# Optimization experiments

Measured on AMD Instinct MI355X. Metric: run time of the kernel, lower is better.

## Reference

```python
import jax, jax.numpy as jnp
import numpy as np

N = 200000      # query points
D_IN = 3        # coordinate dims
H = 256         # hidden features
L = 4           # hidden layers (between first and last Perceptron)
S = 8           # n_series == out_features


def setup_inputs() -> dict:
    key = jax.random.key(0)
    ks = jax.random.split(key, 7)
    coords = jax.random.normal(ks[0], (N, D_IN), dtype=jnp.float32)
    # Stacked per-series weights (all series share shapes; original loads the
    # same checkpoint into each, but we use independent random params).
    scale0 = 1.0 / np.sqrt(D_IN)
    scaleh = 1.0 / np.sqrt(H)
    W0 = jax.random.uniform(ks[1], (S, D_IN, H), jnp.float32, -scale0, scale0)
    b0 = jax.random.uniform(ks[2], (S, H), jnp.float32, -scale0, scale0)
    Wh = jax.random.uniform(ks[3], (S, L, H, H), jnp.float32, -scaleh, scaleh)
    bh = jax.random.uniform(ks[4], (S, L, H), jnp.float32, -scaleh, scaleh)
    Wout = jax.random.uniform(ks[5], (S, H, 1), jnp.float32, -scaleh, scaleh)
    bout = jax.random.uniform(ks[6], (S, 1), jnp.float32, -scaleh, scaleh)
    return {"coords": coords, "W0": W0, "b0": b0, "Wh": Wh, "bh": bh,
            "Wout": Wout, "bout": bout}


def reference(coords, W0, b0, Wh, bh, Wout, bout):
    # All S series' MLPs batched into grouped GEMMs (einsum over series axis s).
    # Perceptron = Linear + softplus; last layer is plain Linear.
    h = jax.nn.softplus(jnp.einsum('nd,sdh->snh', coords, W0) + b0[:, None, :])
    for i in range(L):  # small fixed layer count
        h = jax.nn.softplus(
            jnp.einsum('snh,shk->snk', h, Wh[:, i]) + bh[:, i][:, None, :])
    out = jnp.einsum('snh,sho->sno', h, Wout) + bout[:, None, :]  # [S,N,1]
    output = jnp.transpose(out[..., 0], (1, 0))  # concat along dim=1 -> [N,S]
    return (output, coords)
```

## Files before the change

kernel.cpp:

```cpp
#include <hip/hip_runtime.h>
#include <hip/hip_bf16.h>
#include <cstdint>

typedef __attribute__((ext_vector_type(8))) short short8;
typedef __attribute__((ext_vector_type(4))) float float4v;

#define LOG2E 1.44269504088896340736f
#define LN2   0.69314718055994530942f

#if __has_builtin(__builtin_amdgcn_exp2f)
__device__ __forceinline__ float fexp2(float x){ return __builtin_amdgcn_exp2f(x); }
#else
__device__ __forceinline__ float fexp2(float x){ return exp2f(x); }
#endif
#if __has_builtin(__builtin_amdgcn_logf)
__device__ __forceinline__ float flog2(float x){ return __builtin_amdgcn_logf(x); }
#else
__device__ __forceinline__ float flog2(float x){ return log2f(x); }
#endif

__device__ __forceinline__ float softplus_hat(float zh){
  return flog2(1.0f + fexp2(zh));
}

__device__ __forceinline__ unsigned short bf16_trunc(float f){
  return (unsigned short)(__builtin_bit_cast(unsigned int, f) >> 16);
}

__global__ void convert_wh(const float* __restrict__ Wh,
                           unsigned short* __restrict__ Wt){
  int e = blockIdx.x * 256 + threadIdx.x;
  int n  = e & 255;
  int k  = (e >> 8) & 255;
  int sl = e >> 16;
  float v = Wh[e];
  __hip_bfloat16 h = __float2bfloat16(v);
  Wt[(sl << 16) + ((k >> 5) << 13) + (n << 5) + (k & 31)] =
      __builtin_bit_cast(unsigned short, h);
}

__device__ __forceinline__ void layer_mfma(
    const unsigned short* __restrict__ slab,
    const unsigned short* __restrict__ h_lds,
    int lane, int colb, int q, float4v acc[4][4])
{
  const unsigned short* bbase = slab + (colb << 5) + (q << 3);

  short8 bq[3][4];
  #pragma unroll
  for (int i = 0; i < 3; ++i)
    #pragma unroll
    for (int ni = 0; ni < 4; ++ni)
      bq[i][ni] = *(const short8*)(bbase + (i << 13) + (ni << 9));

  short8 a0[4], a1[4];
  #pragma unroll
  for (int mi = 0; mi < 4; ++mi) {
    int m = mi * 16 + (lane & 15);
    a0[mi] = *(const short8*)&h_lds[m * 256 + ((q ^ (m & 7)) << 3)];
  }

  #pragma unroll
  for (int kb = 0; kb < 8; ++kb) {
    short8* cur = (kb & 1) ? a1 : a0;
    short8* nxt = (kb & 1) ? a0 : a1;
    if (kb < 7) {
      #pragma unroll
      for (int mi = 0; mi < 4; ++mi) {
        int m = mi * 16 + (lane & 15);
        int o = ((kb + 1) << 2) + q;
        nxt[mi] = *(const short8*)&h_lds[m * 256 + ((o ^ (m & 7)) << 3)];
      }
    }
    #pragma unroll
    for (int mi = 0; mi < 4; ++mi)
      #pragma unroll
      for (int ni = 0; ni < 4; ++ni)
        acc[mi][ni] = __builtin_amdgcn_mfma_f32_16x16x32_bf16(
            cur[mi], bq[kb % 3][ni], acc[mi][ni], 0, 0, 0);
    if (kb + 3 < 8) {
      #pragma unroll
      for (int ni = 0; ni < 4; ++ni)
        bq[kb % 3][ni] = *(const short8*)(bbase + ((kb + 3) << 13) + (ni << 9));
    }
  }
}

__global__ __launch_bounds__(256, 2) void series_mlp(
    const float* __restrict__ coords,
    const float* __restrict__ W0, const float* __restrict__ b0,
    const float* __restrict__ bh,
    const float* __restrict__ Wout, const float* __restrict__ bout,
    const unsigned short* __restrict__ Wt,
    float* __restrict__ out)
{
  __shared__ __align__(16) unsigned short h_lds[64 * 256];
  __shared__ float cbuf[192];

  const int tid  = threadIdx.x;
  const int lane = tid & 63;
  const int wave = tid >> 6;
  const int s    = blockIdx.x & 7;
  const int m0   = (blockIdx.x >> 3) * 64;

  if (tid < 192) cbuf[tid] = coords[m0 * 3 + tid];
  __syncthreads();

  {
    const int c  = tid;
    const float w0 = W0[(s * 3 + 0) * 256 + c] * LOG2E;
    const float w1 = W0[(s * 3 + 1) * 256 + c] * LOG2E;
    const float w2 = W0[(s * 3 + 2) * 256 + c] * LOG2E;
    const float bb = b0[s * 256 + c] * LOG2E;
    const int cc = c >> 3, cl = c & 7;
    for (int m = 0; m < 64; ++m) {
      float zh = fmaf(cbuf[m * 3 + 2], w2,
                 fmaf(cbuf[m * 3 + 1], w1,
                 fmaf(cbuf[m * 3 + 0], w0, bb)));
      h_lds[m * 256 + ((cc ^ (m & 7)) << 3) + cl] = bf16_trunc(softplus_hat(zh));
    }
  }
  __syncthreads();

  const int colb = (wave << 6) + (lane & 15);
  const int q    = lane >> 4;

  #pragma unroll
  for (int l = 0; l < 3; ++l) {
    const unsigned short* slab = Wt + (((s << 2) + l) << 16);

    float bias[4];
    #pragma unroll
    for (int ni = 0; ni < 4; ++ni)
      bias[ni] = bh[((s << 2) + l) * 256 + colb + ni * 16] * LOG2E;

    float4v acc[4][4];
    #pragma unroll
    for (int mi = 0; mi < 4; ++mi)
      #pragma unroll
      for (int ni = 0; ni < 4; ++ni)
        acc[mi][ni] = (float4v){bias[ni], bias[ni], bias[ni], bias[ni]};

    layer_mfma(slab, h_lds, lane, colb, q, acc);

    #pragma unroll
    for (int mi = 0; mi < 4; ++mi)
      #pragma unroll
      for (int ni = 0; ni < 4; ++ni) {
        float4v v = acc[mi][ni];
        #pragma unroll
        for (int r = 0; r < 4; ++r) v[r] = softplus_hat(v[r]);
        acc[mi][ni] = v;
      }

    __syncthreads();

    #pragma unroll
    for (int mi = 0; mi < 4; ++mi) {
      #pragma unroll
      for (int ni = 0; ni < 4; ++ni) {
        float4v v = acc[mi][ni];
        int col = (wave << 6) + ni * 16 + (lane & 15);
        int cc = col >> 3, cl = col & 7;
        int mb = mi * 16 + (q << 2);
        #pragma unroll
        for (int r = 0; r < 4; ++r) {
          int m = mb + r;
          h_lds[m * 256 + ((cc ^ (m & 7)) << 3) + cl] = bf16_trunc(v[r]);
        }
      }
    }
    __syncthreads();
  }

  {
    const unsigned short* slab = Wt + (((s << 2) + 3) << 16);

    float bias[4];
    #pragma unroll
    for (int ni = 0; ni < 4; ++ni)
      bias[ni] = bh[((s << 2) + 3) * 256 + colb + ni * 16] * LOG2E;

    float4v acc[4][4];
    #pragma unroll
    for (int mi = 0; mi < 4; ++mi)
      #pragma unroll
      for (int ni = 0; ni < 4; ++ni)
        acc[mi][ni] = (float4v){bias[ni], bias[ni], bias[ni], bias[ni]};

    layer_mfma(slab, h_lds, lane, colb, q, acc);

    float wv[4];
    #pragma unroll
    for (int ni = 0; ni < 4; ++ni)
      wv[ni] = Wout[(s << 8) + colb + ni * 16];
    float p[16];
    #pragma unroll
    for (int i = 0; i < 16; ++i) p[i] = 0.f;
    #pragma unroll
    for (int mi = 0; mi < 4; ++mi)
      #pragma unroll
      for (int ni = 0; ni < 4; ++ni) {
        float4v v = acc[mi][ni];
        #pragma unroll
        for (int r = 0; r < 4; ++r)
          p[mi * 4 + r] = fmaf(softplus_hat(v[r]), wv[ni], p[mi * 4 + r]);
      }

    __syncthreads();
    float* red = (float*)h_lds;
    #pragma unroll
    for (int mi = 0; mi < 4; ++mi)
      #pragma unroll
      for (int r = 0; r < 4; ++r) {
        int row = mi * 16 + (q << 2) + r;
        red[row * 68 + (wave << 4) + (lane & 15)] = p[mi * 4 + r];
      }
    __syncthreads();

    if (tid < 64) {
      const float4v* rr = (const float4v*)&red[tid * 68];
      float4v a = rr[0];
      #pragma unroll
      for (int i = 1; i < 16; ++i) {
        float4v b = rr[i];
        a.x += b.x; a.y += b.y; a.z += b.z; a.w += b.w;
      }
      float tot = (a.x + a.y) + (a.z + a.w);
      out[(m0 + tid) * 8 + s] = fmaf(LN2, tot, bout[s]);
    }
  }
}

__global__ __launch_bounds__(256) void series_mlp_slow(
    const float* __restrict__ coords,
    const float* __restrict__ W0, const float* __restrict__ b0,
    const float* __restrict__ Wh, const float* __restrict__ bh,
    const float* __restrict__ Wout, const float* __restrict__ bout,
    float* __restrict__ out)
{
  __shared__ float h[64 * 256];
  __shared__ float cbuf[192];
  __shared__ float red[256];
  const int tid = threadIdx.x;
  const int s   = blockIdx.y;
  const int m0  = blockIdx.x * 64;

  if (tid < 192) cbuf[tid] = coords[m0 * 3 + tid];
  __syncthreads();
  {
    const float w0 = W0[(s * 3 + 0) * 256 + tid];
    const float w1 = W0[(s * 3 + 1) * 256 + tid];
    const float w2 = W0[(s * 3 + 2) * 256 + tid];
    const float bb = b0[s * 256 + tid];
    for (int m = 0; m < 64; ++m) {
      float z = fmaf(cbuf[m * 3 + 2], w2,
                fmaf(cbuf[m * 3 + 1], w1,
                fmaf(cbuf[m * 3 + 0], w0, bb)));
      h[m * 256 + tid] = LN2 * softplus_hat(z * LOG2E);
    }
  }
  __syncthreads();

  for (int l = 0; l < 4; ++l) {
    const float* W = Wh + (((s << 2) + l) << 16);
    const float bb = bh[((s << 2) + l) * 256 + tid];
    float acc[64];
    #pragma unroll
    for (int m = 0; m < 64; ++m) acc[m] = bb;
    for (int kc = 0; kc < 64; ++kc) {
      float w0 = W[(kc * 4 + 0) * 256 + tid];
      float w1 = W[(kc * 4 + 1) * 256 + tid];
      float w2 = W[(kc * 4 + 2) * 256 + tid];
      float w3 = W[(kc * 4 + 3) * 256 + tid];
      #pragma unroll
      for (int m = 0; m < 64; ++m) {
        float4v hv = *(const float4v*)&h[m * 256 + kc * 4];
        acc[m] = fmaf(hv.w, w3, fmaf(hv.z, w2,
                 fmaf(hv.y, w1, fmaf(hv.x, w0, acc[m]))));
      }
    }
    __syncthreads();
    #pragma unroll
    for (int m = 0; m < 64; ++m)
      h[m * 256 + tid] = LN2 * softplus_hat(acc[m] * LOG2E);
    __syncthreads();
  }
  {
    const int m = tid >> 2, qq = tid & 3;
    const float* wv = Wout + (s << 8);
    float sum = 0.f;
    for (int i = 0; i < 16; ++i) {
      int kk = (qq << 6) + ((((tid & 15) + i) << 2) & 63);
      float4v hv = *(const float4v*)&h[m * 256 + kk];
      sum += hv.x * wv[kk] + hv.y * wv[kk + 1] + hv.z * wv[kk + 2] + hv.w * wv[kk + 3];
    }
    red[tid] = sum;
    __syncthreads();
    if (tid < 64)
      out[(m0 + tid) * 8 + s] =
          red[tid * 4] + red[tid * 4 + 1] + red[tid * 4 + 2] + red[tid * 4 + 3] + bout[s];
  }
}

extern "C" void kernel_launch(void* const* d_in, const int* in_sizes, int n_in,
                              void* d_out, int out_size, void* d_ws, size_t ws_size,
                              hipStream_t stream) {
  const float* coords = (const float*)d_in[0];
  const float* W0     = (const float*)d_in[1];
  const float* b0     = (const float*)d_in[2];
  const float* Wh     = (const float*)d_in[3];
  const float* bh     = (const float*)d_in[4];
  const float* Wout   = (const float*)d_in[5];
  const float* bout   = (const float*)d_in[6];
  float* out = (float*)d_out;

  const size_t WT_BYTES = (size_t)8 * 4 * 256 * 256 * 2;
  if (ws_size >= WT_BYTES) {
    unsigned short* Wt = (unsigned short*)d_ws;
    convert_wh<<<8192, 256, 0, stream>>>(Wh, Wt);
    series_mlp<<<dim3(25000), dim3(256), 0, stream>>>(
        coords, W0, b0, bh, Wout, bout, Wt, out);
  } else {
    series_mlp_slow<<<dim3(3125, 8), dim3(256), 0, stream>>>(
        coords, W0, b0, Wh, bh, Wout, bout, out);
  }
  hipMemcpyAsync(out + (size_t)200000 * 8, coords,
                 (size_t)200000 * 3 * sizeof(float),
                 hipMemcpyDeviceToDevice, stream);
}
```

Before: 1.001 ms.

## Prefetch next layer weights across layers and pad LDS rows instead of XOR swizzle

The weight register ring buffer now persists across hidden layers, so the first three k-blocks of the next layer's weights are loaded during the tail of the current layer's MFMA loop. This hides the global-load latency at each layer start. The XOR-swizzled LDS activation layout is replaced by a padded row stride of 264 elements, which simplifies address arithmetic to constant offsets. The first layer also reads coordinates as float4 vectors. The risks are different LDS bank-conflict behaviour under padding, slightly more LDS use, and higher register pressure from keeping prefetched weights live across layer boundaries.

Measured after the change: 916.0 us. 1.09x faster.

```diff
diff --git a/kernel.cpp b/kernel.cpp
--- a/kernel.cpp
+++ b/kernel.cpp
@@ -27,6 +27,8 @@
   return (unsigned short)(__builtin_bit_cast(unsigned int, f) >> 16);
 }
 
+#define HSTRIDE 264
+
 __global__ void convert_wh(const float* __restrict__ Wh,
                            unsigned short* __restrict__ Wt){
   int e = blockIdx.x * 256 + threadIdx.x;
@@ -39,26 +41,23 @@
       __builtin_bit_cast(unsigned short, h);
 }
 
-__device__ __forceinline__ void layer_mfma(
-    const unsigned short* __restrict__ slab,
-    const unsigned short* __restrict__ h_lds,
-    int lane, int colb, int q, float4v acc[4][4])
+__device__ __forceinline__ float4v bf16_mfma(short8 a, short8 b, float4v c){
+  return __builtin_amdgcn_mfma_f32_16x16x32_bf16(a, b, c, 0, 0, 0);
+}
+
+template<int L>
+__device__ __forceinline__ void hidden_mfma(
+    const unsigned short* __restrict__ bbase0,
+    const unsigned short* __restrict__ aptr,
+    short8 (&bq)[3][4], float4v (&acc)[4][4])
 {
-  const unsigned short* bbase = slab + (colb << 5) + (q << 3);
-
-  short8 bq[3][4];
-  #pragma unroll
-  for (int i = 0; i < 3; ++i)
-    #pragma unroll
-    for (int ni = 0; ni < 4; ++ni)
-      bq[i][ni] = *(const short8*)(bbase + (i << 13) + (ni << 9));
+  const unsigned short* bb = bbase0 + L * 65536;
+  const unsigned short* bn = bbase0 + (L + 1) * 65536;
 
   short8 a0[4], a1[4];
   #pragma unroll
-  for (int mi = 0; mi < 4; ++mi) {
-    int m = mi * 16 + (lane & 15);
-    a0[mi] = *(const short8*)&h_lds[m * 256 + ((q ^ (m & 7)) << 3)];
-  }
+  for (int mi = 0; mi < 4; ++mi)
+    a0[mi] = *(const short8*)(aptr + mi * 4224);
 
   #pragma unroll
   for (int kb = 0; kb < 8; ++kb) {
@@ -66,22 +65,23 @@
     short8* nxt = (kb & 1) ? a0 : a1;
     if (kb < 7) {
       #pragma unroll
-      for (int mi = 0; mi < 4; ++mi) {
-        int m = mi * 16 + (lane & 15);
-        int o = ((kb + 1) << 2) + q;
-        nxt[mi] = *(const short8*)&h_lds[m * 256 + ((o ^ (m & 7)) << 3)];
-      }
-    }
+      for (int mi = 0; mi < 4; ++mi)
+        nxt[mi] = *(const short8*)(aptr + mi * 4224 + (kb + 1) * 32);
+    }
+    const int slot = (8 * L + kb) % 3;
     #pragma unroll
     for (int mi = 0; mi < 4; ++mi)
       #pragma unroll
       for (int ni = 0; ni < 4; ++ni)
-        acc[mi][ni] = __builtin_amdgcn_mfma_f32_16x16x32_bf16(
-            cur[mi], bq[kb % 3][ni], acc[mi][ni], 0, 0, 0);
-    if (kb + 3 < 8) {
+        acc[mi][ni] = bf16_mfma(cur[mi], bq[slot][ni], acc[mi][ni]);
+    if (kb < 5) {
       #pragma unroll
       for (int ni = 0; ni < 4; ++ni)
-        bq[kb % 3][ni] = *(const short8*)(bbase + ((kb + 3) << 13) + (ni << 9));
+        bq[slot][ni] = *(const short8*)(bb + (kb + 3) * 8192 + ni * 512);
+    } else if (L < 3) {
+      #pragma unroll
+      for (int ni = 0; ni < 4; ++ni)
+        bq[slot][ni] = *(const short8*)(bn + (kb - 5) * 8192 + ni * 512);
     }
   }
 }
@@ -94,7 +94,7 @@
     const unsigned short* __restrict__ Wt,
     float* __restrict__ out)
 {
-  __shared__ __align__(16) unsigned short h_lds[64 * 256];
+  __shared__ __align__(16) unsigned short h_lds[64 * HSTRIDE];
   __shared__ float cbuf[192];
 
   const int tid  = threadIdx.x;
@@ -112,83 +112,91 @@
     const float w1 = W0[(s * 3 + 1) * 256 + c] * LOG2E;
     const float w2 = W0[(s * 3 + 2) * 256 + c] * LOG2E;
     const float bb = b0[s * 256 + c] * LOG2E;
-    const int cc = c >> 3, cl = c & 7;
-    for (int m = 0; m < 64; ++m) {
-      float zh = fmaf(cbuf[m * 3 + 2], w2,
-                 fmaf(cbuf[m * 3 + 1], w1,
-                 fmaf(cbuf[m * 3 + 0], w0, bb)));
-      h_lds[m * 256 + ((cc ^ (m & 7)) << 3) + cl] = bf16_trunc(softplus_hat(zh));
+    const float4v* c4 = (const float4v*)cbuf;
+    #pragma unroll
+    for (int j = 0; j < 16; ++j) {
+      float4v x0 = c4[j * 3 + 0];
+      float4v x1 = c4[j * 3 + 1];
+      float4v x2 = c4[j * 3 + 2];
+      float z0 = fmaf(x0.z, w2, fmaf(x0.y, w1, fmaf(x0.x, w0, bb)));
+      float z1 = fmaf(x1.y, w2, fmaf(x1.x, w1, fmaf(x0.w, w0, bb)));
+      float z2 = fmaf(x2.x, w2, fmaf(x1.w, w1, fmaf(x1.z, w0, bb)));
+      float z3 = fmaf(x2.w, w2, fmaf(x2.z, w1, fmaf(x2.y, w0, bb)));
+      h_lds[(4 * j + 0) * HSTRIDE + c] = bf16_trunc(softplus_hat(z0));
+      h_lds[(4 * j + 1) * HSTRIDE + c] = bf16_trunc(softplus_hat(z1));
+      h_lds[(4 * j + 2) * HSTRIDE + c] = bf16_trunc(softplus_hat(z2));
+      h_lds[(4 * j + 3) * HSTRIDE + c] = bf16_trunc(softplus_hat(z3));
     }
   }
   __syncthreads();
 
   const int colb = (wave << 6) + (lane & 15);
   const int q    = lane >> 4;
-
+  const unsigned short* aptr = h_lds + (lane & 15) * HSTRIDE + q * 8;
+  unsigned short* cptr = h_lds + (q * 4) * HSTRIDE + colb;
+
+  const unsigned short* bbase0 = Wt + ((s << 2) << 16) + (colb << 5) + (q << 3);
+
+  short8 bq[3][4];
   #pragma unroll
-  for (int l = 0; l < 3; ++l) {
-    const unsigned short* slab = Wt + (((s << 2) + l) << 16);
-
+  for (int i = 0; i < 3; ++i)
+    #pragma unroll
+    for (int ni = 0; ni < 4; ++ni)
+      bq[i][ni] = *(const short8*)(bbase0 + i * 8192 + ni * 512);
+
+  float4v acc[4][4];
+
+  #define HIDDEN_LAYER(L)                                                     \
+  {                                                                           \
+    float bias[4];                                                            \
+    _Pragma("unroll")                                                         \
+    for (int ni = 0; ni < 4; ++ni)                                            \
+      bias[ni] = bh[((s << 2) + L) * 256 + colb + ni * 16] * LOG2E;           \
+    _Pragma("unroll")                                                         \
+    for (int mi = 0; mi < 4; ++mi)                                            \
+      _Pragma("unroll")                                                       \
+      for (int ni = 0; ni < 4; ++ni)                                          \
+        acc[mi][ni] = (float4v){bias[ni], bias[ni], bias[ni], bias[ni]};      \
+    hidden_mfma<L>(bbase0, aptr, bq, acc);                                    \
+    _Pragma("unroll")                                                         \
+    for (int mi = 0; mi < 4; ++mi)                                            \
+      _Pragma("unroll")                                                       \
+      for (int ni = 0; ni < 4; ++ni) {                                        \
+        float4v v = acc[mi][ni];                                              \
+        _Pragma("unroll")                                                     \
+        for (int r = 0; r < 4; ++r) v[r] = softplus_hat(v[r]);                \
+        acc[mi][ni] = v;                                                      \
+      }                                                                       \
+    __syncthreads();                                                          \
+    _Pragma("unroll")                                                         \
+    for (int mi = 0; mi < 4; ++mi)                                            \
+      _Pragma("unroll")                                                       \
+      for (int ni = 0; ni < 4; ++ni) {                                        \
+        float4v v = acc[mi][ni];                                              \
+        _Pragma("unroll")                                                     \
+        for (int r = 0; r < 4; ++r)                                           \
+          cptr[mi * 4224 + r * HSTRIDE + ni * 16] = bf16_trunc(v[r]);         \
+      }                                                                       \
+    __syncthreads();                                                          \
+  }
+
+  HIDDEN_LAYER(0)
+  HIDDEN_LAYER(1)
+  HIDDEN_LAYER(2)
+  #undef HIDDEN_LAYER
+
+  {
     float bias[4];
     #pragma unroll
     for (int ni = 0; ni < 4; ++ni)
-      bias[ni] = bh[((s << 2) + l) * 256 + colb + ni * 16] * LOG2E;
-
-    float4v acc[4][4];
+      bias[ni] = bh[((s << 2) + 3) * 256 + colb + ni * 16] * LOG2E;
     #pragma unroll
     for (int mi = 0; mi < 4; ++mi)
       #pragma unroll
       for (int ni = 0; ni < 4; ++ni)
         acc[mi][ni] = (float4v){bias[ni], bias[ni], bias[ni], bias[ni]};
 
-    layer_mfma(slab, h_lds, lane, colb, q, acc);
-
-    #pragma unroll
-    for (int mi = 0; mi < 4; ++mi)
-      #pragma unroll
-      for (int ni = 0; ni < 4; ++ni) {
-        float4v v = acc[mi][ni];
-        #pragma unroll
-        for (int r = 0; r < 4; ++r) v[r] = softplus_hat(v[r]);
-        acc[mi][ni] = v;
-      }
-
-    __syncthreads();
-
-    #pragma unroll
-    for (int mi = 0; mi < 4; ++mi) {
-      #pragma unroll
-      for (int ni = 0; ni < 4; ++ni) {
-        float4v v = acc[mi][ni];
-        int col = (wave << 6) + ni * 16 + (lane & 15);
-        int cc = col >> 3, cl = col & 7;
-        int mb = mi * 16 + (q << 2);
-        #pragma unroll
-        for (int r = 0; r < 4; ++r) {
-          int m = mb + r;
-          h_lds[m * 256 + ((cc ^ (m & 7)) << 3) + cl] = bf16_trunc(v[r]);
-        }
-      }
-    }
-    __syncthreads();
-  }
-
-  {
-    const unsigned short* slab = Wt + (((s << 2) + 3) << 16);
-
-    float bias[4];
-    #pragma unroll
-    for (int ni = 0; ni < 4; ++ni)
-      bias[ni] = bh[((s << 2) + 3) * 256 + colb + ni * 16] * LOG2E;
-
-    float4v acc[4][4];
-    #pragma unroll
-    for (int mi = 0; mi < 4; ++mi)
-      #pragma unroll
-      for (int ni = 0; ni < 4; ++ni)
-        acc[mi][ni] = (float4v){bias[ni], bias[ni], bias[ni], bias[ni]};
-
-    layer_mfma(slab, h_lds, lane, colb, q, acc);
+    hidden_mfma<3>(bbase0, aptr, bq, acc);
 
     float wv[4];
     #pragma unroll
```

## Ping-pong two row tiles per block to overlap MFMA with softplus epilogue

Applied to the files above, without the earlier changes.

Each block now owns two 64-row tiles held in two LDS buffers. Each phase runs one tile's layer GEMM while applying softplus and the bf16 store, or the output dot product, to the other tile's accumulators, so transcendental work interleaves with MFMA issue. The weight prefetch ring now runs continuously across layer boundaries, and the LDS activation layout changes from an XOR-swizzled row-major layout to a chunk-major one. The grid is halved, one tile is computed twice, and register pressure doubles because two accumulator sets stay live.

Measured after the change: 947.0 us. -5.4%, faster.

```diff
diff --git a/kernel.cpp b/kernel.cpp
--- a/kernel.cpp
+++ b/kernel.cpp
@@ -39,26 +39,37 @@
       __builtin_bit_cast(unsigned short, h);
 }
 
-__device__ __forceinline__ void layer_mfma(
-    const unsigned short* __restrict__ slab,
-    const unsigned short* __restrict__ h_lds,
-    int lane, int colb, int q, float4v acc[4][4])
+__device__ __forceinline__ float4v bf16_mfma(short8 a, short8 b, float4v c){
+  return __builtin_amdgcn_mfma_f32_16x16x32_bf16(a, b, c, 0, 0, 0);
+}
+
+template<int P>
+__device__ __forceinline__ void run_phase(
+    const unsigned short* __restrict__ bbase0,
+    const unsigned short* __restrict__ aS,
+    unsigned short* __restrict__ cO,
+    short8 (&bq)[3][4],
+    float4v (&accS)[4][4], float4v (&accO)[4][4],
+    const float* __restrict__ bh_s, int colb,
+    const float (&wv)[4], float (&pd)[16])
 {
-  const unsigned short* bbase = slab + (colb << 5) + (q << 3);
-
-  short8 bq[3][4];
-  #pragma unroll
-  for (int i = 0; i < 3; ++i)
+  constexpr int LYR = P >> 1;
+  {
+    float bias[4];
     #pragma unroll
     for (int ni = 0; ni < 4; ++ni)
-      bq[i][ni] = *(const short8*)(bbase + (i << 13) + (ni << 9));
+      bias[ni] = bh_s[LYR * 256 + colb + ni * 16] * LOG2E;
+    #pragma unroll
+    for (int mi = 0; mi < 4; ++mi)
+      #pragma unroll
+      for (int ni = 0; ni < 4; ++ni)
+        accS[mi][ni] = (float4v){bias[ni], bias[ni], bias[ni], bias[ni]};
+  }
 
   short8 a0[4], a1[4];
   #pragma unroll
-  for (int mi = 0; mi < 4; ++mi) {
-    int m = mi * 16 + (lane & 15);
-    a0[mi] = *(const short8*)&h_lds[m * 256 + ((q ^ (m & 7)) << 3)];
-  }
+  for (int mi = 0; mi < 4; ++mi)
+    a0[mi] = *(const short8*)(aS + mi * 128);
 
   #pragma unroll
   for (int kb = 0; kb < 8; ++kb) {
@@ -66,22 +77,42 @@
     short8* nxt = (kb & 1) ? a0 : a1;
     if (kb < 7) {
       #pragma unroll
-      for (int mi = 0; mi < 4; ++mi) {
-        int m = mi * 16 + (lane & 15);
-        int o = ((kb + 1) << 2) + q;
-        nxt[mi] = *(const short8*)&h_lds[m * 256 + ((o ^ (m & 7)) << 3)];
+      for (int mi = 0; mi < 4; ++mi)
+        nxt[mi] = *(const short8*)(aS + (kb + 1) * 2048 + mi * 128);
+    }
+    const int slot = (8 * P + kb) % 3;
+    #pragma unroll
+    for (int mi = 0; mi < 4; ++mi)
+      #pragma unroll
+      for (int ni = 0; ni < 4; ++ni)
+        accS[mi][ni] = bf16_mfma(cur[mi], bq[slot][ni], accS[mi][ni]);
+
+    if constexpr (P >= 1 && P < 7) {
+      #pragma unroll
+      for (int g = 2 * kb; g < 2 * kb + 2; ++g) {
+        const int mi = g >> 2, ni = g & 3;
+        float4v v = accO[mi][ni];
+        #pragma unroll
+        for (int r = 0; r < 4; ++r)
+          cO[ni * 1024 + mi * 128 + r * 8] = bf16_trunc(softplus_hat(v[r]));
       }
-    }
-    #pragma unroll
-    for (int mi = 0; mi < 4; ++mi)
+    } else if constexpr (P == 7) {
+      #pragma unroll
+      for (int g = 2 * kb; g < 2 * kb + 2; ++g) {
+        const int mi = g >> 2, ni = g & 3;
+        float4v v = accO[mi][ni];
+        #pragma unroll
+        for (int r = 0; r < 4; ++r)
+          pd[mi * 4 + r] = fmaf(softplus_hat(v[r]), wv[ni], pd[mi * 4 + r]);
+      }
+    }
+
+    const int x = 8 * P + kb + 3;
+    if (x <= 63) {
+      const int XL = x >> 4, xkb = x & 7;
       #pragma unroll
       for (int ni = 0; ni < 4; ++ni)
-        acc[mi][ni] = __builtin_amdgcn_mfma_f32_16x16x32_bf16(
-            cur[mi], bq[kb % 3][ni], acc[mi][ni], 0, 0, 0);
-    if (kb + 3 < 8) {
-      #pragma unroll
-      for (int ni = 0; ni < 4; ++ni)
-        bq[kb % 3][ni] = *(const short8*)(bbase + ((kb + 3) << 13) + (ni << 9));
+        bq[slot][ni] = *(const short8*)(bbase0 + XL * 65536 + xkb * 8192 + ni * 512);
     }
   }
 }
@@ -94,141 +125,113 @@
     const unsigned short* __restrict__ Wt,
     float* __restrict__ out)
 {
-  __shared__ __align__(16) unsigned short h_lds[64 * 256];
-  __shared__ float cbuf[192];
+  __shared__ __align__(16) unsigned short h[2][16384];
 
   const int tid  = threadIdx.x;
   const int lane = tid & 63;
-  const int wave = tid >> 6;
+  const int wn   = tid >> 6;
   const int s    = blockIdx.x & 7;
-  const int m0   = (blockIdx.x >> 3) * 64;
-
-  if (tid < 192) cbuf[tid] = coords[m0 * 3 + tid];
-  __syncthreads();
+  const int mblk = blockIdx.x >> 3;
+  const int m0A  = mblk * 64;
+  const int m0B  = (mblk + 1562) * 64;
+
+  const int colb = (wn << 6) + (lane & 15);
+  const int q    = lane >> 4;
+
+  const unsigned short* bbase0 = Wt + ((s << 2) << 16) + (colb << 5) + (q << 3);
+
+  short8 bq[3][4];
+  #pragma unroll
+  for (int i = 0; i < 3; ++i)
+    #pragma unroll
+    for (int ni = 0; ni < 4; ++ni)
+      bq[i][ni] = *(const short8*)(bbase0 + i * 8192 + ni * 512);
 
   {
-    const int c  = tid;
+    const int c = tid;
     const float w0 = W0[(s * 3 + 0) * 256 + c] * LOG2E;
     const float w1 = W0[(s * 3 + 1) * 256 + c] * LOG2E;
     const float w2 = W0[(s * 3 + 2) * 256 + c] * LOG2E;
     const float bb = b0[s * 256 + c] * LOG2E;
-    const int cc = c >> 3, cl = c & 7;
+    unsigned short* hA = &h[0][(c >> 3) * 512 + (c & 7)];
+    unsigned short* hB = &h[1][(c >> 3) * 512 + (c & 7)];
+    const float* cpA = coords + m0A * 3;
+    const float* cpB = coords + m0B * 3;
+    #pragma unroll 8
     for (int m = 0; m < 64; ++m) {
-      float zh = fmaf(cbuf[m * 3 + 2], w2,
-                 fmaf(cbuf[m * 3 + 1], w1,
-                 fmaf(cbuf[m * 3 + 0], w0, bb)));
-      h_lds[m * 256 + ((cc ^ (m & 7)) << 3) + cl] = bf16_trunc(softplus_hat(zh));
-    }
-  }
-  __syncthreads();
-
-  const int colb = (wave << 6) + (lane & 15);
-  const int q    = lane >> 4;
-
-  #pragma unroll
-  for (int l = 0; l < 3; ++l) {
-    const unsigned short* slab = Wt + (((s << 2) + l) << 16);
-
-    float bias[4];
-    #pragma unroll
-    for (int ni = 0; ni < 4; ++ni)
-      bias[ni] = bh[((s << 2) + l) * 256 + colb + ni * 16] * LOG2E;
-
-    float4v acc[4][4];
-    #pragma unroll
-    for (int mi = 0; mi < 4; ++mi)
-      #pragma unroll
-      for (int ni = 0; ni < 4; ++ni)
-        acc[mi][ni] = (float4v){bias[ni], bias[ni], bias[ni], bias[ni]};
-
-    layer_mfma(slab, h_lds, lane, colb, q, acc);
-
-    #pragma unroll
-    for (int mi = 0; mi < 4; ++mi)
-      #pragma unroll
-      for (int ni = 0; ni < 4; ++ni) {
-        float4v v = acc[mi][ni];
-        #pragma unroll
-        for (int r = 0; r < 4; ++r) v[r] = softplus_hat(v[r]);
-        acc[mi][ni] = v;
-      }
-
-    __syncthreads();
-
-    #pragma unroll
-    for (int mi = 0; mi < 4; ++mi) {
-      #pragma unroll
-      for (int ni = 0; ni < 4; ++ni) {
-        float4v v = acc[mi][ni];
-        int col = (wave << 6) + ni * 16 + (lane & 15);
-        int cc = col >> 3, cl = col & 7;
-        int mb = mi * 16 + (q << 2);
-        #pragma unroll
-        for (int r = 0; r < 4; ++r) {
-          int m = mb + r;
-          h_lds[m * 256 + ((cc ^ (m & 7)) << 3) + cl] = bf16_trunc(v[r]);
-        }
-      }
-    }
-    __syncthreads();
-  }
-
-  {
-    const unsigned short* slab = Wt + (((s << 2) + 3) << 16);
-
-    float bias[4];
-    #pragma unroll
-    for (int ni = 0; ni < 4; ++ni)
-      bias[ni] = bh[((s << 2) + 3) * 256 + colb + ni * 16] * LOG2E;
-
-    float4v acc[4][4];
-    #pragma unroll
-    for (int mi = 0; mi < 4; ++mi)
-      #pragma unroll
-      for (int ni = 0; ni < 4; ++ni)
-        acc[mi][ni] = (float4v){bias[ni], bias[ni], bias[ni], bias[ni]};
-
-    layer_mfma(slab, h_lds, lane, colb, q, acc);
-
-    float wv[4];
-    #pragma unroll
-    for (int ni = 0; ni < 4; ++ni)
-      wv[ni] = Wout[(s << 8) + colb + ni * 16];
-    float p[16];
-    #pragma unroll
-    for (int i = 0; i < 16; ++i) p[i] = 0.f;
-    #pragma unroll
-    for (int mi = 0; mi < 4; ++mi)
-      #pragma unroll
-      for (int ni = 0; ni < 4; ++ni) {
-        float4v v = acc[mi][ni];
-        #pragma unroll
-        for (int r = 0; r < 4; ++r)
-          p[mi * 4 + r] = fmaf(softplus_hat(v[r]), wv[ni], p[mi * 4 + r]);
-      }
-
-    __syncthreads();
-    float* red = (float*)h_lds;
-    #pragma unroll
-    for (int mi = 0; mi < 4; ++mi)
-      #pragma unroll
-      for (int r = 0; r < 4; ++r) {
-        int row = mi * 16 + (q << 2) + r;
-        red[row * 68 + (wave << 4) + (lane & 15)] = p[mi * 4 + r];
-      }
-    __syncthreads();
-
-    if (tid < 64) {
-      const float4v* rr = (const float4v*)&red[tid * 68];
-      float4v a = rr[0];
-      #pragma unroll
-      for (int i = 1; i < 16; ++i) {
-        float4v b = rr[i];
-        a.x += b.x; a.y += b.y; a.z += b.z; a.w += b.w;
-      }
-      float tot = (a.x + a.y) + (a.z + a.w);
-      out[(m0 + tid) * 8 + s] = fmaf(LN2, tot, bout[s]);
-    }
+      float zA = fmaf(cpA[3*m+2], w2, fmaf(cpA[3*m+1], w1, fmaf(cpA[3*m], w0, bb)));
+      float zB = fmaf(cpB[3*m+2], w2, fmaf(cpB[3*m+1], w1, fmaf(cpB[3*m], w0, bb)));
+      hA[m * 8] = bf16_trunc(softplus_hat(zA));
+      hB[m * 8] = bf16_trunc(softplus_hat(zB));
+    }
+  }
+  __syncthreads();
+
+  const unsigned short* aA = &h[0][q * 512 + (lane & 15) * 8];
+  const unsigned short* aB = &h[1][q * 512 + (lane & 15) * 8];
+  unsigned short* cA = &h[0][(colb >> 3) * 512 + (colb & 7) + q * 32];
+  unsigned short* cB = &h[1][(colb >> 3) * 512 + (colb & 7) + q * 32];
+
+  float wv[4];
+  #pragma unroll
+  for (int ni = 0; ni < 4; ++ni) wv[ni] = Wout[(s << 8) + colb + ni * 16];
+  const float* bh_s = bh + (s << 10);
+
+  float4v accA[4][4], accB[4][4];
+  float pd[16];
+  #pragma unroll
+  for (int i = 0; i < 16; ++i) pd[i] = 0.f;
+
+  run_phase<0>(bbase0, aA, cB, bq, accA, accB, bh_s, colb, wv, pd); __syncthreads();
+  run_phase<1>(bbase0, aB, cA, bq, accB, accA, bh_s, colb, wv, pd); __syncthreads();
+  run_phase<2>(bbase0, aA, cB, bq, accA, accB, bh_s, colb, wv, pd); __syncthreads();
+  run_phase<3>(bbase0, aB, cA, bq, accB, accA, bh_s, colb, wv, pd); __syncthreads();
+  run_phase<4>(bbase0, aA, cB, bq, accA, accB, bh_s, colb, wv, pd); __syncthreads();
+  run_phase<5>(bbase0, aB, cA, bq, accB, accA, bh_s, colb, wv, pd); __syncthreads();
+  run_phase<6>(bbase0, aA, cB, bq, accA, accB, bh_s, colb, wv, pd); __syncthreads();
+  run_phase<7>(bbase0, aB, cA, bq, accB, accA, bh_s, colb, wv, pd);
+
+  float* redA = (float*)&h[0][0];
+  #pragma unroll
+  for (int mi = 0; mi < 4; ++mi)
+    #pragma unroll
+    for (int r = 0; r < 4; ++r)
+      redA[(mi * 16 + q * 4 + r) * 68 + (wn << 4) + (lane & 15)] = pd[mi * 4 + r];
+  __syncthreads();
+
+  float pd2[16];
+  #pragma unroll
+  for (int i = 0; i < 16; ++i) pd2[i] = 0.f;
+  #pragma unroll
+  for (int mi = 0; mi < 4; ++mi)
+    #pragma unroll
+    for (int ni = 0; ni < 4; ++ni) {
+      float4v v = accB[mi][ni];
+      #pragma unroll
+      for (int r = 0; r < 4; ++r)
+        pd2[mi * 4 + r] = fmaf(softplus_hat(v[r]), wv[ni], pd2[mi * 4 + r]);
+    }
+  float* redB = (float*)&h[1][0];
+  #pragma unroll
+  for (int mi = 0; mi < 4; ++mi)
+    #pragma unroll
+    for (int r = 0; r < 4; ++r)
+      redB[(mi * 16 + q * 4 + r) * 68 + (wn << 4) + (lane & 15)] = pd2[mi * 4 + r];
+  __syncthreads();
+
+  if (tid < 128) {
+    const int t = tid >> 6, r = tid & 63;
+    const float* red = t ? (const float*)&h[1][0] : (const float*)&h[0][0];
+    const float4v* rr = (const float4v*)&red[r * 68];
+    float4v a = rr[0];
+    #pragma unroll
+    for (int i = 1; i < 16; ++i) {
+      float4v b = rr[i];
+      a.x += b.x; a.y += b.y; a.z += b.z; a.w += b.w;
+    }
+    float tot = (a.x + a.y) + (a.z + a.w);
+    const int m0 = t ? m0B : m0A;
+    out[(m0 + r) * 8 + s] = fmaf(LN2, tot, bout[s]);
   }
 }
 
@@ -239,7 +242,7 @@
     const float* __restrict__ Wout, const float* __restrict__ bout,
     float* __restrict__ out)
 {
-  __shared__ float h[64 * 256];
+  __shared__ float hh[64 * 256];
   __shared__ float cbuf[192];
   __shared__ float red[256];
   const int tid = threadIdx.x;
@@ -257,7 +260,7 @@
       float z = fmaf(cbuf[m * 3 + 2], w2,
                 fmaf(cbuf[m * 3 + 1], w1,
                 fmaf(cbuf[m * 3 + 0], w0, bb)));
-      h[m * 256 + tid] = LN2 * softplus_hat(z * LOG2E);
+      hh[m * 256 + tid] = LN2 * softplus_hat(z * LOG2E);
     }
   }
   __syncthreads();
@@ -275,7 +278,7 @@
       float w3 = W[(kc * 4 + 3) * 256 + tid];
       #pragma unroll
       for (int m = 0; m < 64; ++m) {
-        float4v hv = *(const float4v*)&h[m * 256 + kc * 4];
+        float4v hv = *(const float4v*)&hh[m * 256 + kc * 4];
         acc[m] = fmaf(hv.w, w3, fmaf(hv.z, w2,
                  fmaf(hv.y, w1, fmaf(hv.x, w0, acc[m]))));
       }
@@ -283,7 +286,7 @@
     __syncthreads();
     #pragma unroll
     for (int m = 0; m < 64; ++m)
-      h[m * 256 + tid] = LN2 * softplus_hat(acc[m] * LOG2E);
+      hh[m * 256 + tid] = LN2 * softplus_hat(acc[m] * LOG2E);
     __syncthreads();
   }
   {
@@ -292,7 +295,7 @@
     float sum = 0.f;
     for (int i = 0; i < 16; ++i) {
       int kk = (qq << 6) + ((((tid & 15) + i) << 2) & 63);
-      float4v hv = *(const float4v*)&h[m * 256 + kk];
+      float4v hv = *(const float4v*)&hh[m * 256 + kk];
       sum += hv.x * wv[kk] + hv.y * wv[kk + 1] + hv.z * wv[kk + 2] + hv.w * wv[kk + 3];
     }
     red[tid] = sum;
@@ -319,7 +322,7 @@
   if (ws_size >= WT_BYTES) {
     unsigned short* Wt = (unsigned short*)d_ws;
     convert_wh<<<8192, 256, 0, stream>>>(Wh, Wt);
-    series_mlp<<<dim3(25000), dim3(256), 0, stream>>>(
+    series_mlp<<<dim3(1563 * 8), dim3(256), 0, stream>>>(
         coords, W0, b0, bh, Wout, bout, Wt, out);
   } else {
     series_mlp_slow<<<dim3(3125, 8), dim3(256), 0, stream>>>(
```
